# Performance work log

Hardware: AMD Instinct MI355X
Metric: run time of the kernel (lower is better)

The kernel has to match this reference:

```python
import jax, jax.numpy as jnp
import numpy as np

DIM = 768
NUM_HEADS = 12
HEAD_DIM = DIM // NUM_HEADS
SCALE = HEAD_DIM ** -0.5


def setup_inputs() -> dict:
    key = jax.random.key(0)
    k1, k2, k3 = jax.random.split(key, 3)
    x = jax.random.normal(k1, (32, 577, DIM), dtype=jnp.float32)
    # torch nn.Linear weights are [out_features, in_features]
    W_qkv = jax.random.normal(k2, (3 * DIM, DIM), dtype=jnp.float32) * (DIM ** -0.5)
    W_proj = jax.random.normal(k3, (DIM, DIM), dtype=jnp.float32) * (DIM ** -0.5)
    b_proj = jnp.zeros((DIM,), dtype=jnp.float32)
    return {"x": x, "W_qkv": W_qkv, "W_proj": W_proj, "b_proj": b_proj}


def reference(x, W_qkv, W_proj, b_proj):
    B, N, C = x.shape
    H, D = NUM_HEADS, C // NUM_HEADS
    # qkv: [B, N, 3C] -> [3, B, H, N, D]
    qkv = (x @ W_qkv.T).reshape(B, N, 3, H, D).transpose(2, 0, 3, 1, 4)
    q, k, v = qkv[0], qkv[1], qkv[2]
    attn = jnp.einsum('bhnd,bhmd->bhnm', q, k) * SCALE
    attn = jax.nn.softmax(attn, axis=-1)
    out = jnp.einsum('bhnm,bhmd->bhnd', attn, v)  # [B, H, N, D]
    out = out.transpose(0, 2, 1, 3).reshape(B, N, C)
    return out @ W_proj.T + b_proj
```

## Files before the change

### kernel.cpp

```cpp
#include <hip/hip_runtime.h>
#include <math.h>

#define SEQ    577
#define BATCH  32
#define DIM    768
#define NHEAD  12
#define HDIM   64
#define MROWS  (BATCH * SEQ)
#define QKVN   (3 * DIM)

using half4   = __attribute__((ext_vector_type(4))) _Float16;
using half8   = __attribute__((ext_vector_type(8))) _Float16;
using floatx4 = __attribute__((ext_vector_type(4))) float;

typedef __attribute__((address_space(1))) const unsigned int GU;
typedef __attribute__((address_space(3))) unsigned int LU;

__device__ __forceinline__ void gld_lds16(const _Float16* g, _Float16* l) {
    __builtin_amdgcn_global_load_lds((const GU*)g, (LU*)l, 16, 0, 0);
}

__device__ __forceinline__ unsigned lds_addr(const void* p) {
    return (unsigned)(size_t)(LU*)p;
}

__global__ void cvt3_f32_f16(const float* __restrict__ a, _Float16* __restrict__ ao, int na4,
                             const float* __restrict__ b, _Float16* __restrict__ bo, int nb4,
                             const float* __restrict__ c, _Float16* __restrict__ co, int nc4)
{
    int i = blockIdx.x * blockDim.x + threadIdx.x;
    int stride = gridDim.x * blockDim.x;
    int total = na4 + nb4 + nc4;
    for (; i < total; i += stride) {
        const float4* src; half4* dst; int j = i;
        if (j < na4)            { src = (const float4*)a; dst = (half4*)ao; }
        else if ((j -= na4) < nb4) { src = (const float4*)b; dst = (half4*)bo; }
        else { j -= nb4;          src = (const float4*)c; dst = (half4*)co; }
        float4 v = src[j];
        half4 h;
        h[0] = (_Float16)v.x; h[1] = (_Float16)v.y;
        h[2] = (_Float16)v.z; h[3] = (_Float16)v.w;
        dst[j] = h;
    }
}

template<int OUT_HALF, int HAS_BIAS, int SCALEQ>
__global__ __launch_bounds__(256) void gemm_f16_lds(
    const _Float16* __restrict__ A, const _Float16* __restrict__ B,
    const float* __restrict__ bias, void* __restrict__ Cp,
    int M, int N, int K, int npm, int npn)
{
    __shared__ _Float16 As[2][128 * 32];
    __shared__ _Float16 Bs[2][128 * 32];

    const int GROUP = 8;
    int pid  = blockIdx.x;
    int ngrp = GROUP * npn;
    int g    = pid / ngrp;
    int fm   = g * GROUP;
    int gm   = npm - fm; if (gm > GROUP) gm = GROUP;
    int pm   = fm + (pid % ngrp) % gm;
    int pn   = (pid % ngrp) / gm;
    const int m0 = pm * 128, n0 = pn * 128;

    const int t    = threadIdx.x, lane = t & 63, wv = t >> 6;
    const int quad = lane >> 4,   ln   = lane & 15;
    const int wm   = wv >> 1,     wn   = wv & 1;

    floatx4 acc[4][4];
#pragma unroll
    for (int mt = 0; mt < 4; mt++)
#pragma unroll
        for (int nt = 0; nt < 4; nt++) acc[mt][nt] = {0.f, 0.f, 0.f, 0.f};

    const int sr = wv * 32 + (lane >> 2);
    const int sc = (lane & 3) * 8;
    int ma0 = m0 + sr;      if (ma0 > M - 1) ma0 = M - 1;
    int ma1 = m0 + sr + 16; if (ma1 > M - 1) ma1 = M - 1;
    const _Float16* Ag0 = A + (size_t)ma0 * K + sc;
    const _Float16* Ag1 = A + (size_t)ma1 * K + sc;
    const _Float16* Bg0 = B + (size_t)(n0 + sr) * K + sc;
    const _Float16* Bg1 = B + (size_t)(n0 + sr + 16) * K + sc;
    _Float16* Al0 = &As[0][sr * 32 + sc];
    _Float16* Al1 = &As[0][(sr + 16) * 32 + sc];
    _Float16* Bl0 = &Bs[0][sr * 32 + sc];
    _Float16* Bl1 = &Bs[0][(sr + 16) * 32 + sc];
    const int PHALF = 128 * 32;

    for (int k0 = 0; k0 < K; k0 += 64) {
        __syncthreads();
#pragma unroll
        for (int p = 0; p < 2; p++) {
            gld_lds16(Ag0 + k0 + p * 32, Al0 + p * PHALF);
            gld_lds16(Ag1 + k0 + p * 32, Al1 + p * PHALF);
            gld_lds16(Bg0 + k0 + p * 32, Bl0 + p * PHALF);
            gld_lds16(Bg1 + k0 + p * 32, Bl1 + p * PHALF);
        }
        __syncthreads();

#pragma unroll
        for (int p = 0; p < 2; p++) {
            half8 af[4], bf[4];
#pragma unroll
            for (int mt = 0; mt < 4; mt++)
                af[mt] = *(const half8*)&As[p][(wm * 64 + mt * 16 + ln) * 32 + quad * 8];
#pragma unroll
            for (int nt = 0; nt < 4; nt++)
                bf[nt] = *(const half8*)&Bs[p][(wn * 64 + nt * 16 + ln) * 32 + quad * 8];
#pragma unroll
            for (int mt = 0; mt < 4; mt++)
#pragma unroll
                for (int nt = 0; nt < 4; nt++)
                    acc[mt][nt] = __builtin_amdgcn_mfma_f32_16x16x32_f16(
                        af[mt], bf[nt], acc[mt][nt], 0, 0, 0);
        }
    }

    float bv[4];
    if constexpr (HAS_BIAS) {
#pragma unroll
        for (int nt = 0; nt < 4; nt++) bv[nt] = bias[n0 + wn * 64 + nt * 16 + ln];
    }
    float*    C32 = (float*)Cp;
    _Float16* C16 = (_Float16*)Cp;
#pragma unroll
    for (int mt = 0; mt < 4; mt++)
#pragma unroll
        for (int r = 0; r < 4; r++) {
            int m = m0 + wm * 64 + mt * 16 + quad * 4 + r;
            if (m < M) {
#pragma unroll
                for (int nt = 0; nt < 4; nt++) {
                    int col = n0 + wn * 64 + nt * 16 + ln;
                    float v = acc[mt][nt][r];
                    if constexpr (HAS_BIAS) v += bv[nt];
                    if constexpr (SCALEQ) { if (col < DIM) v *= 0.18033688f; }
                    if constexpr (OUT_HALF) C16[(size_t)m * N + col] = (_Float16)v;
                    else                    C32[(size_t)m * N + col] = v;
                }
            }
        }
}

__global__ __launch_bounds__(256) void attn_f16(
    const _Float16* __restrict__ qkv, _Float16* __restrict__ outp)
{
    __shared__ _Float16 Ks[64 * 64];
    __shared__ _Float16 Vs[64 * 64];

    const int t    = threadIdx.x, lane = t & 63, wv = t >> 6;
    const int quad = lane >> 4,   ln   = lane & 15;
    const int q0   = blockIdx.x * 128;
    const int hd   = blockIdx.y,  b    = blockIdx.z;
    const _Float16* base = qkv + (size_t)b * SEQ * QKVN;

    half8 qreg[2][2];
#pragma unroll
    for (int qc = 0; qc < 2; qc++) {
        int q = q0 + wv * 32 + qc * 16 + ln; if (q >= SEQ) q = SEQ - 1;
#pragma unroll
        for (int kd = 0; kd < 2; kd++)
            qreg[qc][kd] = *(const half8*)(base + (size_t)q * QKVN + hd * HDIM + kd * 32 + quad * 8);
    }

    float lr[2] = {0.f, 0.f};
    floatx4 o[2][4];
#pragma unroll
    for (int qc = 0; qc < 2; qc++)
#pragma unroll
        for (int dt = 0; dt < 4; dt++) o[qc][dt] = {0.f, 0.f, 0.f, 0.f};

    const unsigned vb = lds_addr(Vs) + lane * 8;

    for (int kt0 = 0; kt0 < 10; kt0++) {
        const int k0 = kt0 * 64;

        uint4 krg[2], vrg[2];
#pragma unroll
        for (int i = 0; i < 2; i++) {
            int C = t + (i << 8);
            int krow = C >> 3, kdc = (C & 7) ^ (krow & 7);
            int nk = k0 + krow; if (nk >= SEQ) nk = SEQ - 1;
            krg[i] = *(const uint4*)(base + (size_t)nk * QKVN + DIM + hd * HDIM + kdc * 8);
            int vkey = ((C >> 7) << 4) + (((C >> 3) & 3) << 2) + ((C >> 1) & 3);
            int vd0  = (((C >> 5) & 3) << 4) + ((C & 1) << 3);
            int nv = k0 + vkey; if (nv >= SEQ) nv = SEQ - 1;
            vrg[i] = *(const uint4*)(base + (size_t)nv * QKVN + 2 * DIM + hd * HDIM + vd0);
        }
        __syncthreads();
#pragma unroll
        for (int i = 0; i < 2; i++) {
            int C = t + (i << 8);
            *(uint4*)&Ks[C << 3] = krg[i];
            *(uint4*)&Vs[C << 3] = vrg[i];
        }
        __syncthreads();

        floatx4 sacc[2][4];
#pragma unroll
        for (int qc = 0; qc < 2; qc++)
#pragma unroll
            for (int mt = 0; mt < 4; mt++) sacc[qc][mt] = {0.f, 0.f, 0.f, 0.f};
        const int xr = ln & 7;
#pragma unroll
        for (int kd = 0; kd < 2; kd++) {
            half8 kf[4];
#pragma unroll
            for (int mt = 0; mt < 4; mt++)
                kf[mt] = *(const half8*)&Ks[(mt * 16 + ln) * 64 + (((kd * 4 + quad) ^ xr) << 3)];
#pragma unroll
            for (int mt = 0; mt < 4; mt++) {
                sacc[0][mt] = __builtin_amdgcn_mfma_f32_16x16x32_f16(kf[mt], qreg[0][kd], sacc[0][mt], 0, 0, 0);
                sacc[1][mt] = __builtin_amdgcn_mfma_f32_16x16x32_f16(kf[mt], qreg[1][kd], sacc[1][mt], 0, 0, 0);
            }
        }

        half4 vf[4][4];
#pragma unroll
        for (int kt = 0; kt < 4; kt++) {
            unsigned a = vb + kt * 2048;
            asm volatile("ds_read_b64_tr_b16 %0, %1 offset:0"    : "=v"(vf[kt][0]) : "v"(a));
            asm volatile("ds_read_b64_tr_b16 %0, %1 offset:512"  : "=v"(vf[kt][1]) : "v"(a));
            asm volatile("ds_read_b64_tr_b16 %0, %1 offset:1024" : "=v"(vf[kt][2]) : "v"(a));
            asm volatile("ds_read_b64_tr_b16 %0, %1 offset:1536" : "=v"(vf[kt][3]) : "v"(a));
        }

        if (k0 + 64 > SEQ) {
#pragma unroll
            for (int mt = 0; mt < 4; mt++)
#pragma unroll
                for (int r = 0; r < 4; r++)
                    if (k0 + mt * 16 + quad * 4 + r >= SEQ) {
                        sacc[0][mt][r] = -3e38f;
                        sacc[1][mt][r] = -3e38f;
                    }
        }

        half4 pf[2][4];
#pragma unroll
        for (int qc = 0; qc < 2; qc++) {
#pragma unroll
            for (int mt = 0; mt < 4; mt++)
#pragma unroll
                for (int r = 0; r < 4; r++) {
                    float p = exp2f(sacc[qc][mt][r]);
                    lr[qc] += p;
                    pf[qc][mt][r] = (_Float16)p;
                }
        }

        asm volatile("s_waitcnt lgkmcnt(0)" ::: "memory");
        __builtin_amdgcn_sched_barrier(0);
#pragma unroll
        for (int kt = 0; kt < 4; kt++) {
#pragma unroll
            for (int dt = 0; dt < 4; dt++) {
                o[0][dt] = __builtin_amdgcn_mfma_f32_16x16x16f16(vf[kt][dt], pf[0][kt], o[0][dt], 0, 0, 0);
                o[1][dt] = __builtin_amdgcn_mfma_f32_16x16x16f16(vf[kt][dt], pf[1][kt], o[1][dt], 0, 0, 0);
            }
        }
    }

#pragma unroll
    for (int qc = 0; qc < 2; qc++) {
        lr[qc] += __shfl_xor(lr[qc], 16);
        lr[qc] += __shfl_xor(lr[qc], 32);
    }

#pragma unroll
    for (int qc = 0; qc < 2; qc++) {
        int q = q0 + wv * 32 + qc * 16 + ln;
        if (q < SEQ) {
            float inv = 1.f / lr[qc];
#pragma unroll
            for (int dt = 0; dt < 4; dt++) {
                half4 hv;
                hv[0] = (_Float16)(o[qc][dt][0] * inv);
                hv[1] = (_Float16)(o[qc][dt][1] * inv);
                hv[2] = (_Float16)(o[qc][dt][2] * inv);
                hv[3] = (_Float16)(o[qc][dt][3] * inv);
                *(half4*)&outp[(size_t)(b * SEQ + q) * DIM + hd * HDIM + dt * 16 + quad * 4] = hv;
            }
        }
    }
}

extern "C" void kernel_launch(void* const* d_in, const int* in_sizes, int n_in,
                              void* d_out, int out_size, void* d_ws, size_t ws_size,
                              hipStream_t stream)
{
    const float* x     = (const float*)d_in[0];
    const float* Wqkv  = (const float*)d_in[1];
    const float* Wproj = (const float*)d_in[2];
    const float* bproj = (const float*)d_in[3];
    float* out = (float*)d_out;

    const size_t NX  = (size_t)MROWS * DIM;
    const size_t NWQ = (size_t)QKVN * DIM;
    const size_t NWP = (size_t)DIM * DIM;

    _Float16* x16    = (_Float16*)d_ws;
    _Float16* Wq16   = x16 + NX;
    _Float16* Wp16   = Wq16 + NWQ;
    _Float16* qkv16  = Wp16 + NWP;
    _Float16* attn16 = qkv16 + (size_t)MROWS * QKVN;

    cvt3_f32_f16<<<2048, 256, 0, stream>>>(x, x16, (int)(NX / 4),
                                           Wqkv, Wq16, (int)(NWQ / 4),
                                           Wproj, Wp16, (int)(NWP / 4));

    {
        int npm = (MROWS + 127) / 128, npn = QKVN / 128;
        gemm_f16_lds<1, 0, 1><<<npm * npn, 256, 0, stream>>>(
            x16, Wq16, nullptr, qkv16, MROWS, QKVN, DIM, npm, npn);
    }

    attn_f16<<<dim3((SEQ + 127) / 128, NHEAD, BATCH), 256, 0, stream>>>(qkv16, attn16);

    {
        int npm = (MROWS + 127) / 128, npn = DIM / 128;
        gemm_f16_lds<0, 1, 0><<<npm * npn, 256, 0, stream>>>(
            attn16, Wp16, bproj, out, MROWS, DIM, DIM, npm, npn);
    }
}
```

Baseline: 374.9 us.

## Double-buffer K/V tiles in LDS with async global-to-LDS prefetch

```diff
diff --git a/kernel.cpp b/kernel.cpp
--- a/kernel.cpp
+++ b/kernel.cpp
@@ -145,8 +145,8 @@
 __global__ __launch_bounds__(256) void attn_f16(
     const _Float16* __restrict__ qkv, _Float16* __restrict__ outp)
 {
-    __shared__ _Float16 Ks[64 * 64];
-    __shared__ _Float16 Vs[64 * 64];
+    __shared__ _Float16 Ks[2][64 * 64];
+    __shared__ _Float16 Vs[2][64 * 64];
 
     const int t    = threadIdx.x, lane = t & 63, wv = t >> 6;
     const int quad = lane >> 4,   ln   = lane & 15;
@@ -163,6 +163,13 @@
             qreg[qc][kd] = *(const half8*)(base + (size_t)q * QKVN + hd * HDIM + kd * 32 + quad * 8);
     }
 
+    const int krow = t >> 3;
+    const int kdc  = (t & 7) ^ (krow & 7);
+    const int vkey = ((t >> 7) << 4) + (((t >> 3) & 3) << 2) + ((t >> 1) & 3);
+    const int vd0  = (((t >> 5) & 3) << 4) + ((t & 1) << 3);
+    const _Float16* kcst = base + DIM     + hd * HDIM + kdc * 8;
+    const _Float16* vcst = base + 2 * DIM + hd * HDIM + vd0;
+
     float lr[2] = {0.f, 0.f};
     floatx4 o[2][4];
 #pragma unroll
@@ -170,31 +177,31 @@
 #pragma unroll
         for (int dt = 0; dt < 4; dt++) o[qc][dt] = {0.f, 0.f, 0.f, 0.f};
 
-    const unsigned vb = lds_addr(Vs) + lane * 8;
+    const unsigned vb0 = lds_addr(&Vs[0][0]) + lane * 8;
+
+    gld_lds16(kcst + (size_t)krow * QKVN,        &Ks[0][t * 8]);
+    gld_lds16(kcst + (size_t)(krow + 32) * QKVN, &Ks[0][(t + 256) * 8]);
+    gld_lds16(vcst + (size_t)vkey * QKVN,        &Vs[0][t * 8]);
+    gld_lds16(vcst + (size_t)(vkey + 32) * QKVN, &Vs[0][(t + 256) * 8]);
 
     for (int kt0 = 0; kt0 < 10; kt0++) {
-        const int k0 = kt0 * 64;
-
-        uint4 krg[2], vrg[2];
-#pragma unroll
-        for (int i = 0; i < 2; i++) {
-            int C = t + (i << 8);
-            int krow = C >> 3, kdc = (C & 7) ^ (krow & 7);
-            int nk = k0 + krow; if (nk >= SEQ) nk = SEQ - 1;
-            krg[i] = *(const uint4*)(base + (size_t)nk * QKVN + DIM + hd * HDIM + kdc * 8);
-            int vkey = ((C >> 7) << 4) + (((C >> 3) & 3) << 2) + ((C >> 1) & 3);
-            int vd0  = (((C >> 5) & 3) << 4) + ((C & 1) << 3);
-            int nv = k0 + vkey; if (nv >= SEQ) nv = SEQ - 1;
-            vrg[i] = *(const uint4*)(base + (size_t)nv * QKVN + 2 * DIM + hd * HDIM + vd0);
-        }
+        const int cur = kt0 & 1;
+        const int k0  = kt0 * 64;
+
         __syncthreads();
-#pragma unroll
-        for (int i = 0; i < 2; i++) {
-            int C = t + (i << 8);
-            *(uint4*)&Ks[C << 3] = krg[i];
-            *(uint4*)&Vs[C << 3] = vrg[i];
-        }
-        __syncthreads();
+
+        if (kt0 < 9) {
+            const int k1 = k0 + 64, nb = cur ^ 1;
+            int r0 = k1 + krow;      if (r0 > SEQ - 1) r0 = SEQ - 1;
+            int r1 = k1 + krow + 32; if (r1 > SEQ - 1) r1 = SEQ - 1;
+            int s0 = k1 + vkey;      if (s0 > SEQ - 1) s0 = SEQ - 1;
+            int s1 = k1 + vkey + 32; if (s1 > SEQ - 1) s1 = SEQ - 1;
+            gld_lds16(kcst + (size_t)r0 * QKVN, &Ks[nb][t * 8]);
+            gld_lds16(kcst + (size_t)r1 * QKVN, &Ks[nb][(t + 256) * 8]);
+            gld_lds16(vcst + (size_t)s0 * QKVN, &Vs[nb][t * 8]);
+            gld_lds16(vcst + (size_t)s1 * QKVN, &Vs[nb][(t + 256) * 8]);
+        }
+        __builtin_amdgcn_sched_barrier(0);
 
         floatx4 sacc[2][4];
 #pragma unroll
@@ -207,7 +214,7 @@
             half8 kf[4];
 #pragma unroll
             for (int mt = 0; mt < 4; mt++)
-                kf[mt] = *(const half8*)&Ks[(mt * 16 + ln) * 64 + (((kd * 4 + quad) ^ xr) << 3)];
+                kf[mt] = *(const half8*)&Ks[cur][(mt * 16 + ln) * 64 + (((kd * 4 + quad) ^ xr) << 3)];
 #pragma unroll
             for (int mt = 0; mt < 4; mt++) {
                 sacc[0][mt] = __builtin_amdgcn_mfma_f32_16x16x32_f16(kf[mt], qreg[0][kd], sacc[0][mt], 0, 0, 0);
@@ -216,6 +223,7 @@
         }
 
         half4 vf[4][4];
+        const unsigned vb = vb0 + (cur << 13);
 #pragma unroll
         for (int kt = 0; kt < 4; kt++) {
             unsigned a = vb + kt * 2048;
```

New measurement: 338.1 us. -9.8%, faster.
